# Performance work log

Hardware: AMD Instinct MI355X
Metric: run time of the kernel (lower is better)

Reference implementation:

```python
import jax, jax.numpy as jnp
import numpy as np

B, A, T = 256, 512, 21
DIM = 128
SC = 6
NHEAD, HD = 4, DIM // 4

def conv1d_relu(x, w, b, stride=2):
    # x: (N, C, L), w: (O, I, K)
    y = jax.lax.conv_general_dilated(x, w, (stride,), 'SAME', dimension_numbers=('NCH', 'OIH', 'NCH'))
    return jax.nn.relu(y + b[None, :, None])

def to_vector(feat, vm):
    vec_mask = vm[..., :-1] & vm[..., 1:]
    while vec_mask.ndim < feat.ndim:
        vec_mask = vec_mask[..., None]
    return jnp.where(vec_mask, feat[:, :, 1:] - feat[:, :, :-1], jnp.zeros_like(feat[:, :, 1:]))

def setup_inputs():
    key = jax.random.key(0)
    ks = jax.random.split(key, 24)
    f32 = jnp.float32
    inp = {}
    inp['position'] = jax.random.normal(ks[0], (B, A, T, 2), f32)
    inp['heading'] = jax.random.normal(ks[1], (B, A, T), f32)
    inp['velocity'] = jax.random.normal(ks[2], (B, A, T, 2), f32)
    inp['shape'] = jax.random.uniform(ks[3], (B, A, T, 2), f32)
    inp['current_state'] = jax.random.normal(ks[4], (B, SC), f32)
    inp['category'] = jax.random.randint(ks[5], (B, A), 0, 4)
    inp['valid_mask'] = jax.random.randint(ks[6], (B, A, T), 0, 2).astype(bool)
    # history encoder (CNN) params: 9 -> 32 -> 64 -> 128 channels, k=3, stride 2
    inp['conv1_w'] = jax.random.normal(ks[7], (32, 9, 3), f32) * 0.1
    inp['conv1_b'] = jnp.zeros((32,), f32)
    inp['conv2_w'] = jax.random.normal(ks[8], (64, 32, 3), f32) * 0.1
    inp['conv2_b'] = jnp.zeros((64,), f32)
    inp['conv3_w'] = jax.random.normal(ks[9], (128, 64, 3), f32) * 0.1
    inp['conv3_b'] = jnp.zeros((128,), f32)
    # StateAttentionEncoder params
    inp['se_w'] = jax.random.normal(ks[10], (SC, DIM), f32) * 0.02   # per-channel Linear(1,dim) weights
    inp['se_b'] = jnp.zeros((SC, DIM), f32)
    inp['pos_embed'] = jax.random.normal(ks[11], (1, SC, DIM), f32) * 0.02
    inp['query'] = jax.random.normal(ks[12], (1, 1, DIM), f32) * 0.02
    inp['in_proj_w'] = jax.random.normal(ks[13], (3 * DIM, DIM), f32) * (1.0 / np.sqrt(DIM))
    inp['in_proj_b'] = jnp.zeros((3 * DIM,), f32)
    inp['out_proj_w'] = jax.random.normal(ks[14], (DIM, DIM), f32) * (1.0 / np.sqrt(DIM))
    inp['out_proj_b'] = jnp.zeros((DIM,), f32)
    inp['type_emb'] = jax.random.normal(ks[15], (4, DIM), f32) * 0.02
    return inp

def reference(position, heading, velocity, shape, current_state, category, valid_mask,
              conv1_w, conv1_b, conv2_w, conv2_b, conv3_w, conv3_b,
              se_w, se_b, pos_embed, query, in_proj_w, in_proj_b, out_proj_w, out_proj_b,
              type_emb):
    # --- build per-step agent features (B, A, T-1, 9) ---
    heading_vec = to_vector(heading, valid_mask)
    valid_mask_vec = valid_mask[..., 1:] & valid_mask[..., :-1]
    agent_feature = jnp.concatenate([
        to_vector(position, valid_mask),
        to_vector(velocity, valid_mask),
        jnp.stack([jnp.cos(heading_vec), jnp.sin(heading_vec)], axis=-1),
        shape[:, :, 1:],
        valid_mask_vec.astype(jnp.float32)[..., None],
    ], axis=-1)
    bs, nA, Tm1, C = agent_feature.shape
    x = agent_feature.reshape(bs * nA, Tm1, C).transpose(0, 2, 1)  # (N, 9, T-1)
    # --- history CNN encoder (applied to all rows, then masked; same math as boolean gather/scatter) ---
    h = conv1d_relu(x, conv1_w, conv1_b)
    h = conv1d_relu(h, conv2_w, conv2_b)
    h = conv1d_relu(h, conv3_w, conv3_b)
    enc = h.mean(axis=-1)  # (N, DIM)
    valid_agent = valid_mask.any(-1).reshape(-1)
    x_agent = jnp.where(valid_agent[:, None], enc, 0.0).reshape(bs, nA, DIM)
    # --- ego state attention encoder (eval mode: no token dropout) ---
    ego = current_state[:, :SC]
    x_embed = ego[:, :, None] * se_w[None] + se_b[None] + pos_embed  # (B, SC, DIM)
    Wq, Wk, Wv = in_proj_w[:DIM], in_proj_w[DIM:2 * DIM], in_proj_w[2 * DIM:]
    bq, bk, bv = in_proj_b[:DIM], in_proj_b[DIM:2 * DIM], in_proj_b[2 * DIM:]
    q = (query[0, 0] @ Wq.T + bq).reshape(NHEAD, HD)             # (H, D)
    k = (x_embed @ Wk.T + bk).reshape(bs, SC, NHEAD, HD)          # (B, S, H, D)
    v = (x_embed @ Wv.T + bv).reshape(bs, SC, NHEAD, HD)
    scores = jnp.einsum('hd,bshd->bhs', q, k) * (1.0 / np.sqrt(HD))
    attn = jax.nn.softmax(scores, axis=-1)
    o = jnp.einsum('bhs,bshd->bhd', attn, v).reshape(bs, DIM)
    x_ego = o @ out_proj_w.T + out_proj_b                         # (B, DIM)
    x_agent = x_agent.at[:, 0].set(x_ego)
    # --- type embedding add ---
    return x_agent + type_emb[category]
```

## Files before the change

### kernel.cpp

```cpp
#include <hip/hip_runtime.h>
#include <hip/hip_bf16.h>


#define BB 256
#define AAG 512
#define TT 21
#define NAG (BB * AAG)

typedef __hip_bfloat16 bf16;
typedef __attribute__((ext_vector_type(8))) short s8v;
typedef __attribute__((ext_vector_type(4))) float f4v;

__device__ int g_dtype;
__device__ int g_mask_mode;
__device__ __align__(16) short g_w1p[32 * 64];
__device__ __align__(16) short g_w2p[64 * 96];
__device__ __align__(16) short g_w3p[128 * 192];
__device__ __align__(16) float g_b1[32];
__device__ __align__(16) float g_b2[64];
__device__ __align__(16) float g_b3[128];

template <int DT>
__device__ __forceinline__ float ldf(const void* p, long i) {
    if (DT) return __bfloat162float(((const bf16*)p)[i]);
    return ((const float*)p)[i];
}
template <int DT>
__device__ __forceinline__ void stf(void* p, long i, float v) {
    if (DT) ((bf16*)p)[i] = __float2bfloat16(v);
    else    ((float*)p)[i] = v;
}
__device__ __forceinline__ unsigned short f2bu(float x) {
    bf16 b = __float2bfloat16(x);
    union { bf16 b; unsigned short u; } cv; cv.b = b; return cv.u;
}
__device__ __forceinline__ float bu2f(unsigned short u) {
    union { unsigned int i; float f; } cv; cv.i = ((unsigned int)u) << 16; return cv.f;
}
template <int DT>
__device__ __forceinline__ float2 ldf2(const void* p, long i) {
    if (DT) {
        unsigned int u = *(const unsigned int*)((const bf16*)p + i);
        return make_float2(bu2f((unsigned short)(u & 0xffffu)),
                           bu2f((unsigned short)(u >> 16)));
    }
    return *(const float2*)((const float*)p + i);
}
__device__ __forceinline__ bool mask_at(const void* p, long i, int mode) {
    if (mode == 0) return ((const int*)p)[i] != 0;
    if (mode == 1) return ((const unsigned char*)p)[i] != 0;
    if (mode == 2) return ((const float*)p)[i] != 0.f;
    return (((const unsigned short*)p)[i] & 0x7fff) != 0;
}

__global__ void detect_kernel(const unsigned int* __restrict__ pw,
                              const unsigned char* __restrict__ m) {
    __shared__ int cls[4];
    __shared__ int mv;
    __shared__ int good;
    int tid = threadIdx.x;
    if (tid < 4) cls[tid] = 0;
    if (tid == 0) { mv = 0; good = 0; }
    __syncthreads();
    int g = 0;
    for (int i = tid; i < 1024; i += 256) {
        unsigned int w = pw[i];
        unsigned int h0 = w & 0xffffu, h1 = w >> 16;
        unsigned int e0 = (h0 >> 7) & 0xff, e1 = (h1 >> 7) & 0xff;
        if (h0 == 0 || (e0 >= 90 && e0 <= 160)) g++;
        if (h1 == 0 || (e1 >= 90 && e1 <= 160)) g++;
    }
    atomicAdd(&good, g);
    int l0 = 0, l1 = 0, l2 = 0, l3 = 0, lm = 0;
    for (int i = tid; i < 4096; i += 256) {
        int v = m[i];
        if (v) {
            switch (i & 3) { case 0: l0 = 1; break; case 1: l1 = 1; break;
                             case 2: l2 = 1; break; default: l3 = 1; }
            if (v > lm) lm = v;
        }
    }
    if (l0) atomicOr(&cls[0], 1);
    if (l1) atomicOr(&cls[1], 1);
    if (l2) atomicOr(&cls[2], 1);
    if (l3) atomicOr(&cls[3], 1);
    atomicMax(&mv, lm);
    __syncthreads();
    if (tid == 0) {
        g_dtype = (good >= 1740) ? 1 : 0;
        int mode;
        if (!cls[1] && !cls[2] && !cls[3]) mode = 0;
        else if (!cls[0] && !cls[1])       mode = 2;
        else if (mv <= 1)                  mode = 1;
        else                               mode = 3;
        g_mask_mode = mode;
    }
}

template <int DT>
__global__ void prep_weights_kernel(const void* __restrict__ w1, const void* __restrict__ b1,
                                    const void* __restrict__ w2, const void* __restrict__ b2,
                                    const void* __restrict__ w3, const void* __restrict__ b3) {
    if (g_dtype != DT) return;
    int tid = blockIdx.x * blockDim.x + threadIdx.x;
    int nt = gridDim.x * blockDim.x;
    for (int i = tid; i < 32 * 64; i += nt) {
        int oc = i >> 6, k = i & 63, tap = k >> 4, ic = k & 15;
        float v = (tap < 3 && ic < 9) ? ldf<DT>(w1, oc * 27 + ic * 3 + tap) : 0.f;
        g_w1p[i] = (short)f2bu(v);
    }
    for (int i = tid; i < 64 * 96; i += nt) {
        int oc = i / 96, k = i % 96, tap = k >> 5, ic = k & 31;
        g_w2p[i] = (short)f2bu(ldf<DT>(w2, oc * 96 + ic * 3 + tap));
    }
    for (int i = tid; i < 128 * 192; i += nt) {
        int oc = i / 192, k = i % 192, tap = k >> 6, ic = k & 63;
        g_w3p[i] = (short)f2bu(ldf<DT>(w3, oc * 192 + ic * 3 + tap));
    }
    for (int i = tid; i < 32; i += nt) g_b1[i] = ldf<DT>(b1, i);
    for (int i = tid; i < 64; i += nt) g_b2[i] = ldf<DT>(b2, i);
    for (int i = tid; i < 128; i += nt) g_b3[i] = ldf<DT>(b3, i);
}

#define FEAT_RS 24
#define FEAT_AS 568
#define H1_RS 40
#define H1_AS 440
#define H2_RS 72
#define H2_AS 504
#define C3_AS 392
#define OFF_H1 9088
#define OFF_VALID 32256
#define SMEM_BYTES 32320

#define MFMA16(a, b, c) __builtin_amdgcn_mfma_f32_16x16x32_bf16((a), (b), (c), 0, 0, 0)

template <int DT>
__global__ __launch_bounds__(256) void stage1_kernel(
    const void* __restrict__ pos, const void* __restrict__ heading,
    const void* __restrict__ vel, const void* __restrict__ shp,
    const void* __restrict__ vmask, const int* __restrict__ category,
    const void* __restrict__ type_emb, void* __restrict__ out) {
    if (g_dtype != DT) return;
    __shared__ __align__(16) char smem[SMEM_BYTES];
    short* feat = (short*)smem;
    short* h1   = (short*)smem + OFF_H1;
    short* h2   = (short*)smem;
    short* c3   = (short*)smem + OFF_H1;
    int* s_valid = (int*)(smem + OFF_VALID);

    const int tid = threadIdx.x;
    const int wave = tid >> 6, lane = tid & 63;
    const int col = lane & 15, quad = lane >> 4;
    const long agent0 = (long)blockIdx.x * 16;
    const int mode = g_mask_mode;

    if (tid < 16) s_valid[tid] = 0;
    {
        unsigned int* h1u = (unsigned int*)h1;
        h1u[(tid >> 4) * 220 + 200 + (tid & 15)] = 0;
    }
    __syncthreads();

    for (int idx = tid; idx < 16 * 22; idx += 256) {
        int ag = idx / 22, t = idx % 22;
        short* row = feat + ag * FEAT_AS + t * FEAT_RS;
        if (t >= 20) {
            *(uint4*)row = make_uint4(0, 0, 0, 0);
            *(uint4*)(row + 8) = make_uint4(0, 0, 0, 0);
            if (t == 20) {
                long base = (agent0 + ag) * TT + 20;
                if (mask_at(vmask, base, mode)) atomicOr(&s_valid[ag], 1);
            }
        } else {
            long base = (agent0 + ag) * TT + t;
            bool vmt = mask_at(vmask, base, mode);
            if (vmt) atomicOr(&s_valid[ag], 1);
            bool m2 = vmt && mask_at(vmask, base + 1, mode);
            float2 pa = ldf2<DT>(pos, base * 2), pb = ldf2<DT>(pos, base * 2 + 2);
            float2 va = ldf2<DT>(vel, base * 2), vb = ldf2<DT>(vel, base * 2 + 2);
            float hh0 = ldf<DT>(heading, base), hh1 = ldf<DT>(heading, base + 1);
            float2 sv = ldf2<DT>(shp, base * 2 + 2);
            float dh = m2 ? (hh1 - hh0) : 0.f;
            float sn, cn;
            __sincosf(dh, &sn, &cn);
            unsigned int p0 = f2bu(m2 ? pb.x - pa.x : 0.f) | ((unsigned int)f2bu(m2 ? pb.y - pa.y : 0.f) << 16);
            unsigned int p1 = f2bu(m2 ? vb.x - va.x : 0.f) | ((unsigned int)f2bu(m2 ? vb.y - va.y : 0.f) << 16);
            unsigned int p2 = f2bu(cn) | ((unsigned int)f2bu(sn) << 16);
            unsigned int p3 = f2bu(sv.x) | ((unsigned int)f2bu(sv.y) << 16);
            unsigned int p4 = (unsigned int)f2bu(m2 ? 1.f : 0.f);
            *(uint4*)row = make_uint4(p0, p1, p2, p3);
            *(uint4*)(row + 8) = make_uint4(p4, 0, 0, 0);
        }
    }
    __syncthreads();

    {
        int Mt = wave >> 1;
        int oc = Mt * 16 + col;
        s8v a0 = *(const s8v*)(g_w1p + oc * 64 + quad * 8);
        s8v a1 = *(const s8v*)(g_w1p + oc * 64 + 32 + quad * 8);
        int k0 = quad * 8, k1 = 32 + quad * 8;
        int tap0 = k0 >> 4, ic0 = k0 & 15;
        int tap1 = k1 >> 4, ic1 = k1 & 15;
        int ocr = Mt * 16 + quad * 4;
        f4v bia = *(const f4v*)(g_b1 + ocr);
        int ag = col;
        const short* agbase = feat + ag * FEAT_AS;
#pragma unroll
        for (int i = 0; i < 5; i++) {
            int p = (wave & 1) * 5 + i;
            const short* bb = agbase + 2 * p * FEAT_RS;
            s8v b0 = *(const s8v*)(bb + tap0 * FEAT_RS + ic0);
            s8v b1 = *(const s8v*)(bb + tap1 * FEAT_RS + ic1);
            f4v acc = {0.f, 0.f, 0.f, 0.f};
            acc = MFMA16(a0, b0, acc);
            acc = MFMA16(a1, b1, acc);
            unsigned int lo = f2bu(fmaxf(acc[0] + bia[0], 0.f)) | ((unsigned int)f2bu(fmaxf(acc[1] + bia[1], 0.f)) << 16);
            unsigned int hi = f2bu(fmaxf(acc[2] + bia[2], 0.f)) | ((unsigned int)f2bu(fmaxf(acc[3] + bia[3], 0.f)) << 16);
            *(uint2*)(h1 + ag * H1_AS + p * H1_RS + ocr) = make_uint2(lo, hi);
        }
    }
    __syncthreads();

    {
        unsigned int* h2u = (unsigned int*)h2;
        for (int i = tid; i < 1024; i += 256) {
            int a2 = i >> 6, r = (i >> 5) & 1, cc = i & 31;
            h2u[a2 * 252 + r * 216 + cc] = 0;
        }
        int Mt = wave;
        int oc = Mt * 16 + col;
        s8v a[3];
#pragma unroll
        for (int ks = 0; ks < 3; ks++)
            a[ks] = *(const s8v*)(g_w2p + oc * 96 + ks * 32 + quad * 8);
        int ocr = Mt * 16 + quad * 4;
        f4v bia = *(const f4v*)(g_b2 + ocr);
        int ag = col;
#pragma unroll
        for (int p = 0; p < 5; p++) {
            f4v acc = {0.f, 0.f, 0.f, 0.f};
#pragma unroll
            for (int ks = 0; ks < 3; ks++) {
                s8v b = *(const s8v*)(h1 + ag * H1_AS + (2 * p + ks) * H1_RS + quad * 8);
                acc = MFMA16(a[ks], b, acc);
            }
            unsigned int lo = f2bu(fmaxf(acc[0] + bia[0], 0.f)) | ((unsigned int)f2bu(fmaxf(acc[1] + bia[1], 0.f)) << 16);
            unsigned int hi = f2bu(fmaxf(acc[2] + bia[2], 0.f)) | ((unsigned int)f2bu(fmaxf(acc[3] + bia[3], 0.f)) << 16);
            *(uint2*)(h2 + ag * H2_AS + (p + 1) * H2_RS + ocr) = make_uint2(lo, hi);
        }
    }
    __syncthreads();

#pragma unroll
    for (int m2 = 0; m2 < 2; m2++) {
        int Mt = wave * 2 + m2;
        int oc = Mt * 16 + col;
        s8v a[6];
#pragma unroll
        for (int ks = 0; ks < 6; ks++)
            a[ks] = *(const s8v*)(g_w3p + oc * 192 + ks * 32 + quad * 8);
        int ocr = Mt * 16 + quad * 4;
        f4v bia = *(const f4v*)(g_b3 + ocr);
        int ag = col;
#pragma unroll
        for (int p = 0; p < 3; p++) {
            f4v acc = {0.f, 0.f, 0.f, 0.f};
#pragma unroll
            for (int ks = 0; ks < 6; ks++) {
                int kg = ks * 32 + quad * 8;
                int tap = kg >> 6, ic = kg & 63;
                s8v b = *(const s8v*)(h2 + ag * H2_AS + (2 * p + tap) * H2_RS + ic);
                acc = MFMA16(a[ks], b, acc);
            }
            unsigned int lo = f2bu(fmaxf(acc[0] + bia[0], 0.f)) | ((unsigned int)f2bu(fmaxf(acc[1] + bia[1], 0.f)) << 16);
            unsigned int hi = f2bu(fmaxf(acc[2] + bia[2], 0.f)) | ((unsigned int)f2bu(fmaxf(acc[3] + bia[3], 0.f)) << 16);
            *(uint2*)(c3 + ag * C3_AS + p * 128 + ocr) = make_uint2(lo, hi);
        }
    }
    __syncthreads();

    {
        int ag = tid >> 4;
        int ocg = (tid & 15) * 8;
        const short* cb = c3 + ag * C3_AS;
        s8v x0 = *(const s8v*)(cb + ocg);
        s8v x1 = *(const s8v*)(cb + 128 + ocg);
        s8v x2 = *(const s8v*)(cb + 256 + ocg);
        int valid = s_valid[ag];
        long agl = agent0 + ag;
        int cat = category[agl];
        float vals[8];
#pragma unroll
        for (int j = 0; j < 8; j++) {
            float m = (bu2f((unsigned short)x0[j]) + bu2f((unsigned short)x1[j]) +
                       bu2f((unsigned short)x2[j])) * (1.f / 3.f);
            vals[j] = valid ? m : 0.f;
        }
        if (DT) {
            s8v te = *(const s8v*)((const bf16*)type_emb + (long)cat * 128 + ocg);
            s8v o;
#pragma unroll
            for (int j = 0; j < 8; j++)
                o[j] = (short)f2bu(vals[j] + bu2f((unsigned short)te[j]));
            *(s8v*)((bf16*)out + agl * 128 + ocg) = o;
        } else {
            const float4* tep = (const float4*)((const float*)type_emb + (long)cat * 128 + ocg);
            float4 t0 = tep[0], t1 = tep[1];
            float4 o0 = make_float4(vals[0] + t0.x, vals[1] + t0.y, vals[2] + t0.z, vals[3] + t0.w);
            float4 o1 = make_float4(vals[4] + t1.x, vals[5] + t1.y, vals[6] + t1.z, vals[7] + t1.w);
            float4* op = (float4*)((float*)out + agl * 128 + ocg);
            op[0] = o0; op[1] = o1;
        }
    }
}

template <int DT>
__global__ __launch_bounds__(128) void stage2_kernel(
    const void* __restrict__ cs, const int* __restrict__ category,
    const void* __restrict__ se_w, const void* __restrict__ se_b,
    const void* __restrict__ pe, const void* __restrict__ query,
    const void* __restrict__ ipw, const void* __restrict__ ipb,
    const void* __restrict__ opw, const void* __restrict__ opb,
    const void* __restrict__ type_emb, void* __restrict__ out) {
    if (g_dtype != DT) return;
    int b = blockIdx.x, d = threadIdx.x;
    __shared__ float s_xe[6][128];
    __shared__ float s_qu[128];
    __shared__ float s_q[128];
    __shared__ float s_k[6][128];
    __shared__ float s_v[6][128];
    __shared__ float s_att[4][6];
    __shared__ float s_o[128];

    s_qu[d] = ldf<DT>(query, d);
#pragma unroll
    for (int s = 0; s < 6; s++) {
        float ego = ldf<DT>(cs, b * 6 + s);
        s_xe[s][d] = fmaf(ego, ldf<DT>(se_w, s * 128 + d),
                          ldf<DT>(se_b, s * 128 + d) + ldf<DT>(pe, s * 128 + d));
    }
    __syncthreads();

    float accq = ldf<DT>(ipb, d);
    float bk = ldf<DT>(ipb, 128 + d), bv = ldf<DT>(ipb, 256 + d);
    float acck[6], accv[6];
#pragma unroll
    for (int s = 0; s < 6; s++) { acck[s] = bk; accv[s] = bv; }
    for (int e = 0; e < 128; e++) {
        float wqe = ldf<DT>(ipw, (long)d * 128 + e);
        accq = fmaf(s_qu[e], wqe, accq);
        float wke = ldf<DT>(ipw, (long)(128 + d) * 128 + e);
        float wve = ldf<DT>(ipw, (long)(256 + d) * 128 + e);
#pragma unroll
        for (int s = 0; s < 6; s++) {
            float xe = s_xe[s][e];
            acck[s] = fmaf(xe, wke, acck[s]);
            accv[s] = fmaf(xe, wve, accv[s]);
        }
    }
    s_q[d] = accq;
#pragma unroll
    for (int s = 0; s < 6; s++) { s_k[s][d] = acck[s]; s_v[s][d] = accv[s]; }
    __syncthreads();

    if (d < 4) {
        float sc[6];
        float mx = -1e30f;
#pragma unroll
        for (int s = 0; s < 6; s++) {
            float t = 0.f;
            for (int q = 0; q < 32; q++) t = fmaf(s_q[d * 32 + q], s_k[s][d * 32 + q], t);
            t *= 0.17677669529663687f;
            sc[s] = t;
            mx = fmaxf(mx, t);
        }
        float sum = 0.f;
#pragma unroll
        for (int s = 0; s < 6; s++) { sc[s] = expf(sc[s] - mx); sum += sc[s]; }
        float inv = 1.f / sum;
#pragma unroll
        for (int s = 0; s < 6; s++) s_att[d][s] = sc[s] * inv;
    }
    __syncthreads();

    {
        int h = d >> 5;
        float o = 0.f;
#pragma unroll
        for (int s = 0; s < 6; s++) o = fmaf(s_att[h][s], s_v[s][d], o);
        s_o[d] = o;
    }
    __syncthreads();

    float acc = ldf<DT>(opb, d);
    for (int e = 0; e < 128; e++) acc = fmaf(s_o[e], ldf<DT>(opw, (long)d * 128 + e), acc);
    int cat = category[(long)b * AAG];
    stf<DT>(out, (long)b * AAG * 128 + d, acc + ldf<DT>(type_emb, cat * 128 + d));
}

extern "C" void kernel_launch(void* const* d_in, const int* in_sizes, int n_in,
                              void* d_out, int out_size, void* d_ws, size_t ws_size,
                              hipStream_t stream) {
    const void* position      = d_in[0];
    const void* heading       = d_in[1];
    const void* velocity      = d_in[2];
    const void* shape         = d_in[3];
    const void* current_state = d_in[4];
    const int*  category      = (const int*)d_in[5];
    const void* valid_mask    = d_in[6];
    const void* conv1_w = d_in[7];
    const void* conv1_b = d_in[8];
    const void* conv2_w = d_in[9];
    const void* conv2_b = d_in[10];
    const void* conv3_w = d_in[11];
    const void* conv3_b = d_in[12];
    const void* se_w    = d_in[13];
    const void* se_b    = d_in[14];
    const void* pos_embed = d_in[15];
    const void* query     = d_in[16];
    const void* in_proj_w = d_in[17];
    const void* in_proj_b = d_in[18];
    const void* out_proj_w = d_in[19];
    const void* out_proj_b = d_in[20];
    const void* type_emb   = d_in[21];

    hipLaunchKernelGGL(detect_kernel, dim3(1), dim3(256), 0, stream,
                       (const unsigned int*)position, (const unsigned char*)valid_mask);

    hipLaunchKernelGGL(prep_weights_kernel<0>, dim3(64), dim3(256), 0, stream,
                       conv1_w, conv1_b, conv2_w, conv2_b, conv3_w, conv3_b);
    hipLaunchKernelGGL(prep_weights_kernel<1>, dim3(64), dim3(256), 0, stream,
                       conv1_w, conv1_b, conv2_w, conv2_b, conv3_w, conv3_b);

    hipLaunchKernelGGL(stage1_kernel<0>, dim3(NAG / 16), dim3(256), 0, stream,
                       position, heading, velocity, shape, valid_mask, category, type_emb, d_out);
    hipLaunchKernelGGL(stage1_kernel<1>, dim3(NAG / 16), dim3(256), 0, stream,
                       position, heading, velocity, shape, valid_mask, category, type_emb, d_out);

    hipLaunchKernelGGL(stage2_kernel<0>, dim3(BB), dim3(128), 0, stream,
                       current_state, category, se_w, se_b, pos_embed, query,
                       in_proj_w, in_proj_b, out_proj_w, out_proj_b, type_emb, d_out);
    hipLaunchKernelGGL(stage2_kernel<1>, dim3(BB), dim3(128), 0, stream,
                       current_state, category, se_w, se_b, pos_embed, query,
                       in_proj_w, in_proj_b, out_proj_w, out_proj_b, type_emb, d_out);
}
```

Before: 304.5 us.

## Make each wave own four agents end-to-end and drop block barriers

Stage 1 is restructured so each wave handles its own 4 agents through feature build, all three conv layers and the mean. The MFMA N dimension is remapped to (position, agent) pairs, which removes every __syncthreads between stages. The dtype-templated kernels now branch on g_dtype at runtime inside a single kernel, so half the launches go away. The cost is some wasted MFMA columns and clamped padding lanes, plus the weight fragments for all output tiles now being loaded per wave.

```diff
diff --git a/kernel.cpp b/kernel.cpp
--- a/kernel.cpp
+++ b/kernel.cpp
@@ -98,10 +98,9 @@
 }
 
 template <int DT>
-__global__ void prep_weights_kernel(const void* __restrict__ w1, const void* __restrict__ b1,
-                                    const void* __restrict__ w2, const void* __restrict__ b2,
-                                    const void* __restrict__ w3, const void* __restrict__ b3) {
-    if (g_dtype != DT) return;
+__device__ __forceinline__ void prep_body(const void* w1, const void* b1,
+                                          const void* w2, const void* b2,
+                                          const void* w3, const void* b3) {
     int tid = blockIdx.x * blockDim.x + threadIdx.x;
     int nt = gridDim.x * blockDim.x;
     for (int i = tid; i < 32 * 64; i += nt) {
@@ -122,60 +121,66 @@
     for (int i = tid; i < 128; i += nt) g_b3[i] = ldf<DT>(b3, i);
 }
 
+__global__ void prep_weights_kernel(const void* __restrict__ w1, const void* __restrict__ b1,
+                                    const void* __restrict__ w2, const void* __restrict__ b2,
+                                    const void* __restrict__ w3, const void* __restrict__ b3) {
+    if (g_dtype) prep_body<1>(w1, b1, w2, b2, w3, b3);
+    else         prep_body<0>(w1, b1, w2, b2, w3, b3);
+}
+
 #define FEAT_RS 24
 #define FEAT_AS 568
 #define H1_RS 40
 #define H1_AS 440
 #define H2_RS 72
 #define H2_AS 504
-#define C3_AS 392
+#define C3_RS 144
 #define OFF_H1 9088
 #define OFF_VALID 32256
 #define SMEM_BYTES 32320
 
 #define MFMA16(a, b, c) __builtin_amdgcn_mfma_f32_16x16x32_bf16((a), (b), (c), 0, 0, 0)
 
-template <int DT>
-__global__ __launch_bounds__(256) void stage1_kernel(
-    const void* __restrict__ pos, const void* __restrict__ heading,
-    const void* __restrict__ vel, const void* __restrict__ shp,
-    const void* __restrict__ vmask, const int* __restrict__ category,
-    const void* __restrict__ type_emb, void* __restrict__ out) {
-    if (g_dtype != DT) return;
-    __shared__ __align__(16) char smem[SMEM_BYTES];
-    short* feat = (short*)smem;
-    short* h1   = (short*)smem + OFF_H1;
-    short* h2   = (short*)smem;
-    short* c3   = (short*)smem + OFF_H1;
-    int* s_valid = (int*)(smem + OFF_VALID);
-
+__device__ __forceinline__ uint2 pack_relu(f4v acc, f4v bia) {
+    unsigned int lo = f2bu(fmaxf(acc[0] + bia[0], 0.f)) | ((unsigned int)f2bu(fmaxf(acc[1] + bia[1], 0.f)) << 16);
+    unsigned int hi = f2bu(fmaxf(acc[2] + bia[2], 0.f)) | ((unsigned int)f2bu(fmaxf(acc[3] + bia[3], 0.f)) << 16);
+    return make_uint2(lo, hi);
+}
+
+template <int DT>
+__device__ __forceinline__ void stage1_body(
+    const void* pos, const void* heading, const void* vel, const void* shp,
+    const void* vmask, const int* category, const void* type_emb, void* out,
+    char* smem) {
     const int tid = threadIdx.x;
     const int wave = tid >> 6, lane = tid & 63;
     const int col = lane & 15, quad = lane >> 4;
     const long agent0 = (long)blockIdx.x * 16;
     const int mode = g_mask_mode;
 
-    if (tid < 16) s_valid[tid] = 0;
+    int* s_valid = (int*)(smem + OFF_VALID);
+    short* feat = (short*)smem + wave * 4 * FEAT_AS;
+    short* h1   = (short*)smem + OFF_H1 + wave * 4 * H1_AS;
+    short* h2   = feat;
+    short* c3   = h1;
+
+    if (lane < 4) s_valid[wave * 4 + lane] = 0;
     {
         unsigned int* h1u = (unsigned int*)h1;
-        h1u[(tid >> 4) * 220 + 200 + (tid & 15)] = 0;
-    }
-    __syncthreads();
-
-    for (int idx = tid; idx < 16 * 22; idx += 256) {
+        h1u[(lane >> 4) * 220 + 200 + (lane & 15)] = 0;
+    }
+
+    for (int idx = lane; idx < 88; idx += 64) {
         int ag = idx / 22, t = idx % 22;
         short* row = feat + ag * FEAT_AS + t * FEAT_RS;
+        long base = (agent0 + wave * 4 + ag) * TT + t;
         if (t >= 20) {
             *(uint4*)row = make_uint4(0, 0, 0, 0);
             *(uint4*)(row + 8) = make_uint4(0, 0, 0, 0);
-            if (t == 20) {
-                long base = (agent0 + ag) * TT + 20;
-                if (mask_at(vmask, base, mode)) atomicOr(&s_valid[ag], 1);
-            }
+            if (t == 20 && mask_at(vmask, base, mode)) atomicOr(&s_valid[wave * 4 + ag], 1);
         } else {
-            long base = (agent0 + ag) * TT + t;
             bool vmt = mask_at(vmask, base, mode);
-            if (vmt) atomicOr(&s_valid[ag], 1);
+            if (vmt) atomicOr(&s_valid[wave * 4 + ag], 1);
             bool m2 = vmt && mask_at(vmask, base + 1, mode);
             float2 pa = ldf2<DT>(pos, base * 2), pb = ldf2<DT>(pos, base * 2 + 2);
             float2 va = ldf2<DT>(vel, base * 2), vb = ldf2<DT>(vel, base * 2 + 2);
@@ -193,103 +198,111 @@
             *(uint4*)(row + 8) = make_uint4(p4, 0, 0, 0);
         }
     }
-    __syncthreads();
-
-    {
-        int Mt = wave >> 1;
-        int oc = Mt * 16 + col;
-        s8v a0 = *(const s8v*)(g_w1p + oc * 64 + quad * 8);
-        s8v a1 = *(const s8v*)(g_w1p + oc * 64 + 32 + quad * 8);
+
+    {
+        s8v a00 = *(const s8v*)(g_w1p + col * 64 + quad * 8);
+        s8v a01 = *(const s8v*)(g_w1p + col * 64 + 32 + quad * 8);
+        s8v a10 = *(const s8v*)(g_w1p + (16 + col) * 64 + quad * 8);
+        s8v a11 = *(const s8v*)(g_w1p + (16 + col) * 64 + 32 + quad * 8);
+        f4v bia0 = *(const f4v*)(g_b1 + quad * 4);
+        f4v bia1 = *(const f4v*)(g_b1 + 16 + quad * 4);
         int k0 = quad * 8, k1 = 32 + quad * 8;
         int tap0 = k0 >> 4, ic0 = k0 & 15;
         int tap1 = k1 >> 4, ic1 = k1 & 15;
-        int ocr = Mt * 16 + quad * 4;
-        f4v bia = *(const f4v*)(g_b1 + ocr);
-        int ag = col;
-        const short* agbase = feat + ag * FEAT_AS;
-#pragma unroll
-        for (int i = 0; i < 5; i++) {
-            int p = (wave & 1) * 5 + i;
-            const short* bb = agbase + 2 * p * FEAT_RS;
+#pragma unroll
+        for (int nt = 0; nt < 3; nt++) {
+            int n = nt * 16 + col;
+            int p = n >> 2, ag = n & 3;
+            int pg = p > 9 ? 9 : p;
+            const short* bb = feat + ag * FEAT_AS + 2 * pg * FEAT_RS;
             s8v b0 = *(const s8v*)(bb + tap0 * FEAT_RS + ic0);
             s8v b1 = *(const s8v*)(bb + tap1 * FEAT_RS + ic1);
+            f4v acc0 = {0.f, 0.f, 0.f, 0.f}, acc1 = {0.f, 0.f, 0.f, 0.f};
+            acc0 = MFMA16(a00, b0, acc0); acc0 = MFMA16(a01, b1, acc0);
+            acc1 = MFMA16(a10, b0, acc1); acc1 = MFMA16(a11, b1, acc1);
+            if (p < 10) {
+                short* wr = h1 + ag * H1_AS + p * H1_RS + quad * 4;
+                *(uint2*)wr = pack_relu(acc0, bia0);
+                *(uint2*)(wr + 16) = pack_relu(acc1, bia1);
+            }
+        }
+    }
+
+    {
+        unsigned int* h2u = (unsigned int*)h2;
+#pragma unroll
+        for (int j = 0; j < 4; j++)
+            h2u[j * 252 + (lane >> 5) * 216 + (lane & 31)] = 0;
+    }
+
+    {
+        int p0 = col >> 2, ag0 = col & 3;
+        int n1 = 16 + col;
+        int p1 = n1 >> 2, ag1 = n1 & 3;
+        int pg1 = p1 > 4 ? 4 : p1;
+#pragma unroll
+        for (int Mt = 0; Mt < 4; Mt++) {
+            s8v a0 = *(const s8v*)(g_w2p + (Mt * 16 + col) * 96 + quad * 8);
+            s8v a1 = *(const s8v*)(g_w2p + (Mt * 16 + col) * 96 + 32 + quad * 8);
+            s8v a2 = *(const s8v*)(g_w2p + (Mt * 16 + col) * 96 + 64 + quad * 8);
+            f4v bia = *(const f4v*)(g_b2 + Mt * 16 + quad * 4);
+            {
+                const short* bb = h1 + ag0 * H1_AS + 2 * p0 * H1_RS + quad * 8;
+                f4v acc = {0.f, 0.f, 0.f, 0.f};
+                acc = MFMA16(a0, *(const s8v*)(bb), acc);
+                acc = MFMA16(a1, *(const s8v*)(bb + H1_RS), acc);
+                acc = MFMA16(a2, *(const s8v*)(bb + 2 * H1_RS), acc);
+                *(uint2*)(h2 + ag0 * H2_AS + (p0 + 1) * H2_RS + Mt * 16 + quad * 4) =
+                    pack_relu(acc, bia);
+            }
+            {
+                const short* bb = h1 + ag1 * H1_AS + 2 * pg1 * H1_RS + quad * 8;
+                f4v acc = {0.f, 0.f, 0.f, 0.f};
+                acc = MFMA16(a0, *(const s8v*)(bb), acc);
+                acc = MFMA16(a1, *(const s8v*)(bb + H1_RS), acc);
+                acc = MFMA16(a2, *(const s8v*)(bb + 2 * H1_RS), acc);
+                if (p1 == 4)
+                    *(uint2*)(h2 + ag1 * H2_AS + (p1 + 1) * H2_RS + Mt * 16 + quad * 4) =
+                        pack_relu(acc, bia);
+            }
+        }
+    }
+
+    {
+        int p = col >> 2, ag = col & 3;
+        int pg = p > 2 ? 2 : p;
+        s8v b[6];
+#pragma unroll
+        for (int ks = 0; ks < 6; ks++) {
+            int kg = ks * 32 + quad * 8;
+            int tap = kg >> 6, ic = kg & 63;
+            b[ks] = *(const s8v*)(h2 + ag * H2_AS + (2 * pg + tap) * H2_RS + ic);
+        }
+#pragma unroll
+        for (int Mt = 0; Mt < 8; Mt++) {
             f4v acc = {0.f, 0.f, 0.f, 0.f};
-            acc = MFMA16(a0, b0, acc);
-            acc = MFMA16(a1, b1, acc);
-            unsigned int lo = f2bu(fmaxf(acc[0] + bia[0], 0.f)) | ((unsigned int)f2bu(fmaxf(acc[1] + bia[1], 0.f)) << 16);
-            unsigned int hi = f2bu(fmaxf(acc[2] + bia[2], 0.f)) | ((unsigned int)f2bu(fmaxf(acc[3] + bia[3], 0.f)) << 16);
-            *(uint2*)(h1 + ag * H1_AS + p * H1_RS + ocr) = make_uint2(lo, hi);
-        }
-    }
-    __syncthreads();
-
-    {
-        unsigned int* h2u = (unsigned int*)h2;
-        for (int i = tid; i < 1024; i += 256) {
-            int a2 = i >> 6, r = (i >> 5) & 1, cc = i & 31;
-            h2u[a2 * 252 + r * 216 + cc] = 0;
-        }
-        int Mt = wave;
-        int oc = Mt * 16 + col;
-        s8v a[3];
-#pragma unroll
-        for (int ks = 0; ks < 3; ks++)
-            a[ks] = *(const s8v*)(g_w2p + oc * 96 + ks * 32 + quad * 8);
-        int ocr = Mt * 16 + quad * 4;
-        f4v bia = *(const f4v*)(g_b2 + ocr);
-        int ag = col;
-#pragma unroll
-        for (int p = 0; p < 5; p++) {
-            f4v acc = {0.f, 0.f, 0.f, 0.f};
-#pragma unroll
-            for (int ks = 0; ks < 3; ks++) {
-                s8v b = *(const s8v*)(h1 + ag * H1_AS + (2 * p + ks) * H1_RS + quad * 8);
-                acc = MFMA16(a[ks], b, acc);
+#pragma unroll
+            for (int ks = 0; ks < 6; ks++) {
+                s8v a = *(const s8v*)(g_w3p + (Mt * 16 + col) * 192 + ks * 32 + quad * 8);
+                acc = MFMA16(a, b[ks], acc);
             }
-            unsigned int lo = f2bu(fmaxf(acc[0] + bia[0], 0.f)) | ((unsigned int)f2bu(fmaxf(acc[1] + bia[1], 0.f)) << 16);
-            unsigned int hi = f2bu(fmaxf(acc[2] + bia[2], 0.f)) | ((unsigned int)f2bu(fmaxf(acc[3] + bia[3], 0.f)) << 16);
-            *(uint2*)(h2 + ag * H2_AS + (p + 1) * H2_RS + ocr) = make_uint2(lo, hi);
-        }
-    }
-    __syncthreads();
-
-#pragma unroll
-    for (int m2 = 0; m2 < 2; m2++) {
-        int Mt = wave * 2 + m2;
-        int oc = Mt * 16 + col;
-        s8v a[6];
-#pragma unroll
-        for (int ks = 0; ks < 6; ks++)
-            a[ks] = *(const s8v*)(g_w3p + oc * 192 + ks * 32 + quad * 8);
-        int ocr = Mt * 16 + quad * 4;
-        f4v bia = *(const f4v*)(g_b3 + ocr);
-        int ag = col;
-#pragma unroll
-        for (int p = 0; p < 3; p++) {
-            f4v acc = {0.f, 0.f, 0.f, 0.f};
-#pragma unroll
-            for (int ks = 0; ks < 6; ks++) {
-                int kg = ks * 32 + quad * 8;
-                int tap = kg >> 6, ic = kg & 63;
-                s8v b = *(const s8v*)(h2 + ag * H2_AS + (2 * p + tap) * H2_RS + ic);
-                acc = MFMA16(a[ks], b, acc);
+            if (p < 3) {
+                f4v bia = *(const f4v*)(g_b3 + Mt * 16 + quad * 4);
+                *(uint2*)(c3 + ag * H1_AS + p * C3_RS + Mt * 16 + quad * 4) =
+                    pack_relu(acc, bia);
             }
-            unsigned int lo = f2bu(fmaxf(acc[0] + bia[0], 0.f)) | ((unsigned int)f2bu(fmaxf(acc[1] + bia[1], 0.f)) << 16);
-            unsigned int hi = f2bu(fmaxf(acc[2] + bia[2], 0.f)) | ((unsigned int)f2bu(fmaxf(acc[3] + bia[3], 0.f)) << 16);
-            *(uint2*)(c3 + ag * C3_AS + p * 128 + ocr) = make_uint2(lo, hi);
-        }
-    }
-    __syncthreads();
-
-    {
-        int ag = tid >> 4;
-        int ocg = (tid & 15) * 8;
-        const short* cb = c3 + ag * C3_AS;
+        }
+    }
+
+    {
+        int ag = lane >> 4;
+        int ocg = (lane & 15) * 8;
+        const short* cb = c3 + ag * H1_AS;
         s8v x0 = *(const s8v*)(cb + ocg);
-        s8v x1 = *(const s8v*)(cb + 128 + ocg);
-        s8v x2 = *(const s8v*)(cb + 256 + ocg);
-        int valid = s_valid[ag];
-        long agl = agent0 + ag;
+        s8v x1 = *(const s8v*)(cb + C3_RS + ocg);
+        s8v x2 = *(const s8v*)(cb + 2 * C3_RS + ocg);
+        int valid = s_valid[wave * 4 + ag];
+        long agl = agent0 + wave * 4 + ag;
         int cat = category[agl];
         float vals[8];
 #pragma unroll
@@ -316,7 +329,97 @@
     }
 }
 
-template <int DT>
+__global__ __launch_bounds__(256) void stage1_kernel(
+    const void* __restrict__ pos, const void* __restrict__ heading,
+    const void* __restrict__ vel, const void* __restrict__ shp,
+    const void* __restrict__ vmask, const int* __restrict__ category,
+    const void* __restrict__ type_emb, void* __restrict__ out) {
+    __shared__ __align__(16) char smem[SMEM_BYTES];
+    if (g_dtype) stage1_body<1>(pos, heading, vel, shp, vmask, category, type_emb, out, smem);
+    else         stage1_body<0>(pos, heading, vel, shp, vmask, category, type_emb, out, smem);
+}
+
+template <int DT>
+__device__ __forceinline__ void stage2_body(
+    const void* cs, const int* category,
+    const void* se_w, const void* se_b, const void* pe, const void* query,
+    const void* ipw, const void* ipb, const void* opw, const void* opb,
+    const void* type_emb, void* out, float* sm) {
+    int b = blockIdx.x, d = threadIdx.x;
+    float* s_xe = sm;
+    float* s_qu = sm + 768;
+    float* s_q  = sm + 896;
+    float* s_k  = sm + 1024;
+    float* s_v  = sm + 1792;
+    float* s_att = sm + 2560;
+    float* s_o  = sm + 2584;
+
+    s_qu[d] = ldf<DT>(query, d);
+#pragma unroll
+    for (int s = 0; s < 6; s++) {
+        float ego = ldf<DT>(cs, b * 6 + s);
+        s_xe[s * 128 + d] = fmaf(ego, ldf<DT>(se_w, s * 128 + d),
+                                 ldf<DT>(se_b, s * 128 + d) + ldf<DT>(pe, s * 128 + d));
+    }
+    __syncthreads();
+
+    float accq = ldf<DT>(ipb, d);
+    float bk = ldf<DT>(ipb, 128 + d), bv = ldf<DT>(ipb, 256 + d);
+    float acck[6], accv[6];
+#pragma unroll
+    for (int s = 0; s < 6; s++) { acck[s] = bk; accv[s] = bv; }
+    for (int e = 0; e < 128; e++) {
+        float wqe = ldf<DT>(ipw, (long)d * 128 + e);
+        accq = fmaf(s_qu[e], wqe, accq);
+        float wke = ldf<DT>(ipw, (long)(128 + d) * 128 + e);
+        float wve = ldf<DT>(ipw, (long)(256 + d) * 128 + e);
+#pragma unroll
+        for (int s = 0; s < 6; s++) {
+            float xe = s_xe[s * 128 + e];
+            acck[s] = fmaf(xe, wke, acck[s]);
+            accv[s] = fmaf(xe, wve, accv[s]);
+        }
+    }
+    s_q[d] = accq;
+#pragma unroll
+    for (int s = 0; s < 6; s++) { s_k[s * 128 + d] = acck[s]; s_v[s * 128 + d] = accv[s]; }
+    __syncthreads();
+
+    if (d < 4) {
+        float sc[6];
+        float mx = -1e30f;
+#pragma unroll
+        for (int s = 0; s < 6; s++) {
+            float t = 0.f;
+            for (int q = 0; q < 32; q++) t = fmaf(s_q[d * 32 + q], s_k[s * 128 + d * 32 + q], t);
+            t *= 0.17677669529663687f;
+            sc[s] = t;
+            mx = fmaxf(mx, t);
+        }
+        float sum = 0.f;
+#pragma unroll
+        for (int s = 0; s < 6; s++) { sc[s] = expf(sc[s] - mx); sum += sc[s]; }
+        float inv = 1.f / sum;
+#pragma unroll
+        for (int s = 0; s < 6; s++) s_att[d * 6 + s] = sc[s] * inv;
+    }
+    __syncthreads();
+
+    {
+        int h = d >> 5;
+        float o = 0.f;
+#pragma unroll
+        for (int s = 0; s < 6; s++) o = fmaf(s_att[h * 6 + s], s_v[s * 128 + d], o);
+        s_o[d] = o;
+    }
+    __syncthreads();
+
+    float acc = ldf<DT>(opb, d);
+    for (int e = 0; e < 128; e++) acc = fmaf(s_o[e], ldf<DT>(opw, (long)d * 128 + e), acc);
+    int cat = category[(long)b * AAG];
+    stf<DT>(out, (long)b * AAG * 128 + d, acc + ldf<DT>(type_emb, cat * 128 + d));
+}
+
 __global__ __launch_bounds__(128) void stage2_kernel(
     const void* __restrict__ cs, const int* __restrict__ category,
     const void* __restrict__ se_w, const void* __restrict__ se_b,
@@ -324,80 +427,9 @@
     const void* __restrict__ ipw, const void* __restrict__ ipb,
     const void* __restrict__ opw, const void* __restrict__ opb,
     const void* __restrict__ type_emb, void* __restrict__ out) {
-    if (g_dtype != DT) return;
-    int b = blockIdx.x, d = threadIdx.x;
-    __shared__ float s_xe[6][128];
-    __shared__ float s_qu[128];
-    __shared__ float s_q[128];
-    __shared__ float s_k[6][128];
-    __shared__ float s_v[6][128];
-    __shared__ float s_att[4][6];
-    __shared__ float s_o[128];
-
-    s_qu[d] = ldf<DT>(query, d);
-#pragma unroll
-    for (int s = 0; s < 6; s++) {
-        float ego = ldf<DT>(cs, b * 6 + s);
-        s_xe[s][d] = fmaf(ego, ldf<DT>(se_w, s * 128 + d),
-                          ldf<DT>(se_b, s * 128 + d) + ldf<DT>(pe, s * 128 + d));
-    }
-    __syncthreads();
-
-    float accq = ldf<DT>(ipb, d);
-    float bk = ldf<DT>(ipb, 128 + d), bv = ldf<DT>(ipb, 256 + d);
-    float acck[6], accv[6];
-#pragma unroll
-    for (int s = 0; s < 6; s++) { acck[s] = bk; accv[s] = bv; }
-    for (int e = 0; e < 128; e++) {
-        float wqe = ldf<DT>(ipw, (long)d * 128 + e);
-        accq = fmaf(s_qu[e], wqe, accq);
-        float wke = ldf<DT>(ipw, (long)(128 + d) * 128 + e);
-        float wve = ldf<DT>(ipw, (long)(256 + d) * 128 + e);
-#pragma unroll
-        for (int s = 0; s < 6; s++) {
-            float xe = s_xe[s][e];
-            acck[s] = fmaf(xe, wke, acck[s]);
-            accv[s] = fmaf(xe, wve, accv[s]);
-        }
-    }
-    s_q[d] = accq;
-#pragma unroll
-    for (int s = 0; s < 6; s++) { s_k[s][d] = acck[s]; s_v[s][d] = accv[s]; }
-    __syncthreads();
-
-    if (d < 4) {
-        float sc[6];
-        float mx = -1e30f;
-#pragma unroll
-        for (int s = 0; s < 6; s++) {
-            float t = 0.f;
-            for (int q = 0; q < 32; q++) t = fmaf(s_q[d * 32 + q], s_k[s][d * 32 + q], t);
-            t *= 0.17677669529663687f;
-            sc[s] = t;
-            mx = fmaxf(mx, t);
-        }
-        float sum = 0.f;
-#pragma unroll
-        for (int s = 0; s < 6; s++) { sc[s] = expf(sc[s] - mx); sum += sc[s]; }
-        float inv = 1.f / sum;
-#pragma unroll
-        for (int s = 0; s < 6; s++) s_att[d][s] = sc[s] * inv;
-    }
-    __syncthreads();
-
-    {
-        int h = d >> 5;
-        float o = 0.f;
-#pragma unroll
-        for (int s = 0; s < 6; s++) o = fmaf(s_att[h][s], s_v[s][d], o);
-        s_o[d] = o;
-    }
-    __syncthreads();
-
-    float acc = ldf<DT>(opb, d);
-    for (int e = 0; e < 128; e++) acc = fmaf(s_o[e], ldf<DT>(opw, (long)d * 128 + e), acc);
-    int cat = category[(long)b * AAG];
-    stf<DT>(out, (long)b * AAG * 128 + d, acc + ldf<DT>(type_emb, cat * 128 + d));
+    __shared__ float sm[2712];
+    if (g_dtype) stage2_body<1>(cs, category, se_w, se_b, pe, query, ipw, ipb, opw, opb, type_emb, out, sm);
+    else         stage2_body<0>(cs, category, se_w, se_b, pe, query, ipw, ipb, opw, opb, type_emb, out, sm);
 }
 
 extern "C" void kernel_launch(void* const* d_in, const int* in_sizes, int n_in,
@@ -429,20 +461,13 @@
     hipLaunchKernelGGL(detect_kernel, dim3(1), dim3(256), 0, stream,
                        (const unsigned int*)position, (const unsigned char*)valid_mask);
 
-    hipLaunchKernelGGL(prep_weights_kernel<0>, dim3(64), dim3(256), 0, stream,
+    hipLaunchKernelGGL(prep_weights_kernel, dim3(64), dim3(256), 0, stream,
                        conv1_w, conv1_b, conv2_w, conv2_b, conv3_w, conv3_b);
-    hipLaunchKernelGGL(prep_weights_kernel<1>, dim3(64), dim3(256), 0, stream,
-                       conv1_w, conv1_b, conv2_w, conv2_b, conv3_w, conv3_b);
-
-    hipLaunchKernelGGL(stage1_kernel<0>, dim3(NAG / 16), dim3(256), 0, stream,
+
+    hipLaunchKernelGGL(stage1_kernel, dim3(NAG / 16), dim3(256), 0, stream,
                        position, heading, velocity, shape, valid_mask, category, type_emb, d_out);
-    hipLaunchKernelGGL(stage1_kernel<1>, dim3(NAG / 16), dim3(256), 0, stream,
-                       position, heading, velocity, shape, valid_mask, category, type_emb, d_out);
-
-    hipLaunchKernelGGL(stage2_kernel<0>, dim3(BB), dim3(128), 0, stream,
+
+    hipLaunchKernelGGL(stage2_kernel, dim3(BB), dim3(128), 0, stream,
                        current_state, category, se_w, se_b, pos_embed, query,
                        in_proj_w, in_proj_b, out_proj_w, out_proj_b, type_emb, d_out);
-    hipLaunchKernelGGL(stage2_kernel<1>, dim3(BB), dim3(128), 0, stream,
-                       current_state, category, se_w, se_b, pos_embed, query,
-                       in_proj_w, in_proj_b, out_proj_w, out_proj_b, type_emb, d_out);
-}
+}
```

After: 446.9 us. +46.8%, slower.
